# Performance work log

Measured on AMD Instinct MI355X. Metric: run time of the kernel, lower is better.

Reference implementation:

```python
import jax, jax.numpy as jnp
import numpy as np
import math

IN_F, OUT_F = 512, 512
N_HEADS, N_SPLITS = 32, 4
N = 1024
DELTA_SCALE = 0.1


def setup_inputs() -> dict:
    key = jax.random.key(0)
    k_x, k_h, k_s, k_w = jax.random.split(key, 4)
    stdv = 1.0 / math.sqrt(OUT_F)
    inputs = {
        "input": jax.random.normal(k_x, (N, IN_F), dtype=jnp.float32),
        "head_ix": jax.random.randint(k_h, (N,), 0, N_HEADS, dtype=jnp.int32),
        "split_ix": jax.random.randint(k_s, (N,), 0, N_SPLITS, dtype=jnp.int32),
        # learned parameters (EmbeddingTensor tables)
        "weight": jax.random.uniform(k_w, (N_HEADS, IN_F, OUT_F), dtype=jnp.float32,
                                     minval=-stdv, maxval=stdv),
        "delta_weight": jnp.zeros((N_HEADS * N_SPLITS, IN_F, OUT_F), dtype=jnp.float32),
        "bias": jnp.zeros((N_HEADS, OUT_F), dtype=jnp.float32),
    }
    return inputs


def reference(input, head_ix, split_ix, weight, delta_weight, bias):
    # per-sample weight: base[head] + 0.1 * delta[head * n_splits + split]
    w = weight[head_ix] + delta_weight[head_ix * N_SPLITS + split_ix] * DELTA_SCALE  # [N, in, out]
    # batched vector-matrix multiply + per-head bias
    return jnp.einsum('ab,abc->ac', input, w) + bias[head_ix]  # [N, out]
```

## Files before the change

### kernel.cpp

```cpp
#include <hip/hip_runtime.h>

#define N_SAMP   1024
#define IN_F     512
#define OUT_F    512
#define N_HEADS  32
#define N_SPLITS 4
#define DELTA_SCALE 0.1f

__device__ __forceinline__ void lds_dma16(const float* g, float* l) {
    __builtin_amdgcn_global_load_lds(
        (const __attribute__((address_space(1))) void*)g,
        (__attribute__((address_space(3))) void*)l, 16, 0, 0);
}

template <int J, bool DELTA>
__global__ __launch_bounds__(256) void lms_pass(
    const float* __restrict__ X, const int* __restrict__ head_ix,
    const int* __restrict__ split_ix, const float* __restrict__ Wt,
    const float* __restrict__ bias, float* __restrict__ out)
{
    constexpr int TILE = 64;
    constexpr int KB   = 64;
    constexpr int CT   = 32;
    constexpr int R    = 8;
    constexpr int Jr   = J / R;
    constexpr int XW   = KB + 4;
    constexpr int Q    = KB / 4;
    constexpr int NISS = (KB * TILE * 4) / (256 * 16);

    __shared__ float Wb[KB * TILE];
    __shared__ float Xb[J * XW];
    __shared__ int   list[N_SAMP];
    __shared__ int   cnt;

    const int g   = blockIdx.y;
    const int c0  = blockIdx.x * TILE;
    const int tid = threadIdx.x;

    if (tid == 0) cnt = 0;
    __syncthreads();
    for (int i = tid; i < N_SAMP; i += 256) {
        const int key = DELTA ? head_ix[i] * N_SPLITS + split_ix[i] : head_ix[i];
        if (key == g) { int p = atomicAdd(&cnt, 1); list[p] = i; }
    }
    __syncthreads();
    const int total = cnt;
    if (total == 0) return;

    const float* Wg = Wt + (size_t)g * (IN_F * OUT_F) + c0;

    const int c    = tid & 31;
    const int r    = tid >> 5;
    const int wave = tid >> 6, lane = tid & 63;

    float2 bv;
    if (!DELTA) bv = *(const float2*)(bias + (size_t)g * OUT_F + c0 + c * 2);

    for (int s0 = 0; s0 < total; s0 += J) {
        const int nc = min(total - s0, J);

        float2 acc[Jr];
#pragma unroll
        for (int j = 0; j < Jr; ++j) { acc[j].x = 0.f; acc[j].y = 0.f; }

        for (int k0 = 0; k0 < IN_F; k0 += KB) {
            __syncthreads();

            for (int i = tid; i < J * Q; i += 256) {
                const int s = i / Q, q = i - s * Q;
                float4 v = make_float4(0.f, 0.f, 0.f, 0.f);
                if (s < nc)
                    v = *(const float4*)(X + (size_t)list[s0 + s] * IN_F + k0 + q * 4);
                *(float4*)(&Xb[s * XW + q * 4]) = v;
            }

            const float* wk = Wg + (size_t)k0 * OUT_F;
#pragma unroll
            for (int it = 0; it < NISS; ++it) {
                const int seg  = it * 4 + wave;
                const int unit = seg * 64 + lane;
                const int row  = unit >> 4;
                const int col  = unit & 15;
                lds_dma16(wk + (size_t)row * OUT_F + col * 4, &Wb[seg * 256]);
            }
            __syncthreads();

            for (int k4 = 0; k4 < KB; k4 += 4) {
                const float2 w0 = *(const float2*)(&Wb[(k4 + 0) * TILE + c * 2]);
                const float2 w1 = *(const float2*)(&Wb[(k4 + 1) * TILE + c * 2]);
                const float2 w2 = *(const float2*)(&Wb[(k4 + 2) * TILE + c * 2]);
                const float2 w3 = *(const float2*)(&Wb[(k4 + 3) * TILE + c * 2]);
#pragma unroll
                for (int j = 0; j < Jr; ++j) {
                    const float4 xv = *(const float4*)(&Xb[(r * Jr + j) * XW + k4]);
                    acc[j].x += xv.x * w0.x; acc[j].y += xv.x * w0.y;
                    acc[j].x += xv.y * w1.x; acc[j].y += xv.y * w1.y;
                    acc[j].x += xv.z * w2.x; acc[j].y += xv.z * w2.y;
                    acc[j].x += xv.w * w3.x; acc[j].y += xv.w * w3.y;
                }
            }
        }

#pragma unroll
        for (int j = 0; j < Jr; ++j) {
            const int s = r * Jr + j;
            if (s < nc) {
                float* op = out + (size_t)list[s0 + s] * OUT_F + c0 + c * 2;
                float2 res;
                if (DELTA) {
                    const float2 cur = *(const float2*)op;
                    res.x = cur.x + DELTA_SCALE * acc[j].x;
                    res.y = cur.y + DELTA_SCALE * acc[j].y;
                } else {
                    res.x = acc[j].x + bv.x;
                    res.y = acc[j].y + bv.y;
                }
                *(float2*)op = res;
            }
        }
    }
}

extern "C" void kernel_launch(void* const* d_in, const int* in_sizes, int n_in,
                              void* d_out, int out_size, void* d_ws, size_t ws_size,
                              hipStream_t stream) {
    const float* X        = (const float*)d_in[0];
    const int*   head_ix  = (const int*)d_in[1];
    const int*   split_ix = (const int*)d_in[2];
    const float* W        = (const float*)d_in[3];
    const float* D        = (const float*)d_in[4];
    const float* bias     = (const float*)d_in[5];
    float*       out      = (float*)d_out;

    dim3 gb(OUT_F / 64, N_HEADS);
    lms_pass<64, false><<<gb, 256, 0, stream>>>(X, head_ix, split_ix, W, bias, out);

    dim3 gd(OUT_F / 64, N_HEADS * N_SPLITS);
    lms_pass<16, true><<<gd, 256, 0, stream>>>(X, head_ix, split_ix, D, bias, out);
}
```

Baseline: 270.8 us.

## Stream weights through registers with split-K across threads and LDS reduction

Replaces the LDS-tiled weight staging with direct per-thread register streaming of weight rows, double-buffered in registers. Each thread covers a K slice, and partial sums are reduced through shared memory. It also builds the sample list with a deterministic ballot/popcount compaction instead of atomics, and splits the base pass across two sample-group blocks per head for more parallelism. The aim is to cut barriers and LDS traffic per K step and to raise occupancy. In exchange it adds a reduction phase, larger register arrays (acc[J] with J=32), and reloads the full weight slice once per sample chunk.

Result: faster. 258.9 us (-4.4%).

```diff
diff --git a/kernel.cpp b/kernel.cpp
--- a/kernel.cpp
+++ b/kernel.cpp
@@ -7,113 +7,124 @@
 #define N_SPLITS 4
 #define DELTA_SCALE 0.1f
 
-__device__ __forceinline__ void lds_dma16(const float* g, float* l) {
-    __builtin_amdgcn_global_load_lds(
-        (const __attribute__((address_space(1))) void*)g,
-        (__attribute__((address_space(3))) void*)l, 16, 0, 0);
-}
-
-template <int J, bool DELTA>
-__global__ __launch_bounds__(256) void lms_pass(
+template <int J, bool DELTA, int NSG, int MINW>
+__global__ __launch_bounds__(256, MINW) void lms_stream(
     const float* __restrict__ X, const int* __restrict__ head_ix,
     const int* __restrict__ split_ix, const float* __restrict__ Wt,
     const float* __restrict__ bias, float* __restrict__ out)
 {
-    constexpr int TILE = 64;
-    constexpr int KB   = 64;
-    constexpr int CT   = 32;
-    constexpr int R    = 8;
-    constexpr int Jr   = J / R;
-    constexpr int XW   = KB + 4;
-    constexpr int Q    = KB / 4;
-    constexpr int NISS = (KB * TILE * 4) / (256 * 16);
+    constexpr int KQ   = 8;
+    constexpr int KT   = IN_F / KQ;
+    constexpr int NST  = KT / 4;
+    constexpr int NOUT = (J * 32) / 256;
 
-    __shared__ float Wb[KB * TILE];
-    __shared__ float Xb[J * XW];
+    __shared__ float buf[J * IN_F];
     __shared__ int   list[N_SAMP];
-    __shared__ int   cnt;
+    __shared__ int   wsum[4];
 
-    const int g   = blockIdx.y;
-    const int c0  = blockIdx.x * TILE;
-    const int tid = threadIdx.x;
+    const int g    = blockIdx.y / NSG;
+    const int sg   = blockIdx.y % NSG;
+    const int c0   = blockIdx.x * 64;
+    const int tid  = threadIdx.x;
+    const int c2   = tid & 31;
+    const int kq   = tid >> 5;
+    const int lane = tid & 63;
+    const int wave = tid >> 6;
 
-    if (tid == 0) cnt = 0;
-    __syncthreads();
-    for (int i = tid; i < N_SAMP; i += 256) {
+    int run = 0;
+    for (int r = 0; r < N_SAMP / 256; ++r) {
+        const int i   = r * 256 + tid;
         const int key = DELTA ? head_ix[i] * N_SPLITS + split_ix[i] : head_ix[i];
-        if (key == g) { int p = atomicAdd(&cnt, 1); list[p] = i; }
+        const bool hit = (key == g);
+        const unsigned long long m = __ballot(hit);
+        if (lane == 0) wsum[wave] = __popcll(m);
+        __syncthreads();
+        int base = run;
+        for (int w = 0; w < 4; ++w)
+            if (w < wave) base += wsum[w];
+        if (hit)
+            list[base + __popcll(m & ((1ULL << lane) - 1ULL))] = i;
+        run += wsum[0] + wsum[1] + wsum[2] + wsum[3];
+        __syncthreads();
     }
-    __syncthreads();
-    const int total = cnt;
+    const int total = run;
+    if (total <= sg * J && total > 0) return;
     if (total == 0) return;
 
-    const float* Wg = Wt + (size_t)g * (IN_F * OUT_F) + c0;
+    const float* wp = Wt + (size_t)g * (IN_F * OUT_F)
+                    + (size_t)(kq * KT) * OUT_F + c0 + c2 * 2;
 
-    const int c    = tid & 31;
-    const int r    = tid >> 5;
-    const int wave = tid >> 6, lane = tid & 63;
-
-    float2 bv;
-    if (!DELTA) bv = *(const float2*)(bias + (size_t)g * OUT_F + c0 + c * 2);
-
-    for (int s0 = 0; s0 < total; s0 += J) {
+    for (int s0 = sg * J; s0 < total; s0 += NSG * J) {
         const int nc = min(total - s0, J);
 
-        float2 acc[Jr];
+        __syncthreads();
+        for (int i = tid; i < J * (IN_F / 4); i += 256) {
+            const int s = i >> 7, q = i & 127;
+            float4 v = make_float4(0.f, 0.f, 0.f, 0.f);
+            if (s < nc)
+                v = *(const float4*)(X + (size_t)list[s0 + s] * IN_F + q * 4);
+            *(float4*)(&buf[s * IN_F + q * 4]) = v;
+        }
+        __syncthreads();
+
+        float2 acc[J];
 #pragma unroll
-        for (int j = 0; j < Jr; ++j) { acc[j].x = 0.f; acc[j].y = 0.f; }
+        for (int j = 0; j < J; ++j) { acc[j].x = 0.f; acc[j].y = 0.f; }
 
-        for (int k0 = 0; k0 < IN_F; k0 += KB) {
-            __syncthreads();
+        float2 rb[2][4];
+#pragma unroll
+        for (int u = 0; u < 4; ++u)
+            rb[0][u] = *(const float2*)(wp + (size_t)u * OUT_F);
 
-            for (int i = tid; i < J * Q; i += 256) {
-                const int s = i / Q, q = i - s * Q;
-                float4 v = make_float4(0.f, 0.f, 0.f, 0.f);
-                if (s < nc)
-                    v = *(const float4*)(X + (size_t)list[s0 + s] * IN_F + k0 + q * 4);
-                *(float4*)(&Xb[s * XW + q * 4]) = v;
-            }
+#pragma unroll 2
+        for (int st = 0; st < NST; ++st) {
+            const int nx = (st + 1 < NST) ? st + 1 : NST - 1;
+            const float* wn = wp + (size_t)(nx * 4) * OUT_F;
+            const int nb = (st + 1) & 1, cb = st & 1;
+#pragma unroll
+            for (int u = 0; u < 4; ++u)
+                rb[nb][u] = *(const float2*)(wn + (size_t)u * OUT_F);
 
-            const float* wk = Wg + (size_t)k0 * OUT_F;
+            const float* xb = &buf[kq * KT + st * 4];
 #pragma unroll
-            for (int it = 0; it < NISS; ++it) {
-                const int seg  = it * 4 + wave;
-                const int unit = seg * 64 + lane;
-                const int row  = unit >> 4;
-                const int col  = unit & 15;
-                lds_dma16(wk + (size_t)row * OUT_F + col * 4, &Wb[seg * 256]);
-            }
-            __syncthreads();
-
-            for (int k4 = 0; k4 < KB; k4 += 4) {
-                const float2 w0 = *(const float2*)(&Wb[(k4 + 0) * TILE + c * 2]);
-                const float2 w1 = *(const float2*)(&Wb[(k4 + 1) * TILE + c * 2]);
-                const float2 w2 = *(const float2*)(&Wb[(k4 + 2) * TILE + c * 2]);
-                const float2 w3 = *(const float2*)(&Wb[(k4 + 3) * TILE + c * 2]);
-#pragma unroll
-                for (int j = 0; j < Jr; ++j) {
-                    const float4 xv = *(const float4*)(&Xb[(r * Jr + j) * XW + k4]);
-                    acc[j].x += xv.x * w0.x; acc[j].y += xv.x * w0.y;
-                    acc[j].x += xv.y * w1.x; acc[j].y += xv.y * w1.y;
-                    acc[j].x += xv.z * w2.x; acc[j].y += xv.z * w2.y;
-                    acc[j].x += xv.w * w3.x; acc[j].y += xv.w * w3.y;
-                }
+            for (int j = 0; j < J; ++j) {
+                const float4 xv = *(const float4*)(xb + j * IN_F);
+                acc[j].x += xv.x * rb[cb][0].x; acc[j].y += xv.x * rb[cb][0].y;
+                acc[j].x += xv.y * rb[cb][1].x; acc[j].y += xv.y * rb[cb][1].y;
+                acc[j].x += xv.z * rb[cb][2].x; acc[j].y += xv.z * rb[cb][2].y;
+                acc[j].x += xv.w * rb[cb][3].x; acc[j].y += xv.w * rb[cb][3].y;
             }
         }
 
+        __syncthreads();
+        float2* Red = (float2*)buf;
 #pragma unroll
-        for (int j = 0; j < Jr; ++j) {
-            const int s = r * Jr + j;
-            if (s < nc) {
-                float* op = out + (size_t)list[s0 + s] * OUT_F + c0 + c * 2;
+        for (int j = 0; j < J; ++j)
+            Red[(kq * J + j) * 32 + c2] = acc[j];
+        __syncthreads();
+
+#pragma unroll
+        for (int t = 0; t < NOUT; ++t) {
+            const int oi = t * 256 + tid;
+            const int j = oi >> 5, cc = oi & 31;
+            if (j < nc) {
+                float2 s = make_float2(0.f, 0.f);
+#pragma unroll
+                for (int q = 0; q < KQ; ++q) {
+                    const float2 r = Red[(q * J + j) * 32 + cc];
+                    s.x += r.x; s.y += r.y;
+                }
+                float* op = out + (size_t)list[s0 + j] * OUT_F + c0 + cc * 2;
                 float2 res;
                 if (DELTA) {
                     const float2 cur = *(const float2*)op;
-                    res.x = cur.x + DELTA_SCALE * acc[j].x;
-                    res.y = cur.y + DELTA_SCALE * acc[j].y;
+                    res.x = cur.x + DELTA_SCALE * s.x;
+                    res.y = cur.y + DELTA_SCALE * s.y;
                 } else {
-                    res.x = acc[j].x + bv.x;
-                    res.y = acc[j].y + bv.y;
+                    const float2 bv =
+                        *(const float2*)(bias + (size_t)g * OUT_F + c0 + cc * 2);
+                    res.x = s.x + bv.x;
+                    res.y = s.y + bv.y;
                 }
                 *(float2*)op = res;
             }
@@ -132,9 +143,11 @@
     const float* bias     = (const float*)d_in[5];
     float*       out      = (float*)d_out;
 
-    dim3 gb(OUT_F / 64, N_HEADS);
-    lms_pass<64, false><<<gb, 256, 0, stream>>>(X, head_ix, split_ix, W, bias, out);
+    dim3 gb(OUT_F / 64, N_HEADS * 2);
+    lms_stream<32, false, 2, 2><<<gb, 256, 0, stream>>>(
+        X, head_ix, split_ix, W, bias, out);
 
     dim3 gd(OUT_F / 64, N_HEADS * N_SPLITS);
-    lms_pass<16, true><<<gd, 256, 0, stream>>>(X, head_ix, split_ix, D, bias, out);
+    lms_stream<16, true, 1, 4><<<gd, 256, 0, stream>>>(
+        X, head_ix, split_ix, D, bias, out);
 }
```
